# Kernel tuning notes

Hardware: AMD Instinct MI355X
Metric: run time of the kernel (lower is better)

## Reference

```python
import jax, jax.numpy as jnp
import numpy as np

# Production-scale dims (see shape_source): time-major, batch must be 1.
T, B, D, S, O, M = 1024, 1, 2048, 1024, 512, 48
TANH_BOUND = 10.0
LN_EPS = 1e-5  # haiku LayerNorm default eps


def setup_inputs() -> dict:
    key = jax.random.key(0)
    ks = jax.random.split(key, 8)

    def lin(k, fin, fout):
        return (jax.random.normal(k, (fin, fout), jnp.float32) / np.float32(np.sqrt(fin)))

    lstm_in = D + 2 * O + S  # concat([inp, error, prev_label]) then concat with h
    return {
        "inputs": jax.random.normal(ks[0], (T, B, D), jnp.float32),
        "labels": jax.random.normal(ks[1], (T, B, O), jnp.float32),
        "W_lstm": lin(ks[2], lstm_in, 4 * S),
        "b_lstm": jnp.zeros((4 * S,), jnp.float32),
        "W_write": lin(ks[3], S, 3 * M + 1),
        "b_write": jnp.zeros((3 * M + 1,), jnp.float32),
        "W_read": lin(ks[4], S, 2 * M),
        "b_read": jnp.zeros((2 * M,), jnp.float32),
        "W_rproj": lin(ks[5], M, S),
        "b_rproj": jnp.zeros((S,), jnp.float32),
        "W_out": lin(ks[6], S, O),
        "b_out": jnp.zeros((O,), jnp.float32),
    }


def _fw_memory(inputs, labels, W_lstm, b_lstm, W_write, b_write,
               W_read, b_read, W_rproj, b_rproj, W_out, b_out):
    Bsz = inputs.shape[1]  # must be 1 (jnp.outer key construction)
    slow = W_lstm.shape[1] // 4
    out_size = W_out.shape[1]
    mem = W_rproj.shape[0]

    h0 = jnp.zeros((Bsz, slow), inputs.dtype)
    c0 = jnp.zeros((Bsz, slow), inputs.dtype)
    mem0 = jnp.zeros((mem, mem * mem), inputs.dtype)
    err0 = jnp.zeros((Bsz, out_size), inputs.dtype)
    lab0 = jnp.zeros((Bsz, out_size), inputs.dtype)

    def tick(carry, x):
        h, c, memory, error, prev_label = carry
        inp, label = x  # [B,D], [B,O]
        # --- LSTM (haiku: forget bias +1) ---
        z = jnp.concatenate([inp, error, prev_label], axis=-1)
        gates = jnp.concatenate([z, h], axis=-1) @ W_lstm + b_lstm  # [B,4S]
        i, g, f, o = jnp.split(gates, 4, axis=-1)
        c = jax.nn.sigmoid(f + 1.0) * c + jax.nn.sigmoid(i) * jnp.tanh(g)
        h = jax.nn.sigmoid(o) * jnp.tanh(c)
        out = h
        # --- rank-1 fast-weight write ---
        write = out @ W_write + b_write                 # [B, 3M+1]
        beta = jax.nn.sigmoid(write[:, -1])             # [B]
        k1, k2, v = jnp.split(jnp.tanh(write[:, :-1]), 3, axis=-1)  # [B,M] each
        key_vec = (k1.reshape(-1)[:, None] * k2.reshape(-1)[None, :]).reshape(-1)  # [M^2]
        v_old = memory @ key_vec                        # [M]
        delta = (v - v_old).reshape(-1)                 # [M]
        memory = memory + beta * (delta[:, None] * key_vec[None, :])
        memory = memory / jnp.maximum(1.0, jnp.linalg.norm(memory))
        # --- rank-1 read + LayerNorm (no scale/offset) ---
        r = jnp.tanh(out @ W_read + b_read)             # [B,2M]
        n, e = jnp.split(r, 2, axis=-1)
        read_key = (n.reshape(-1)[:, None] * e.reshape(-1)[None, :]).reshape(-1)  # [M^2]
        nvec = memory @ read_key                        # [M]
        nvec = (nvec - nvec.mean()) / jnp.sqrt(nvec.var() + LN_EPS)
        readout = nvec @ W_rproj + b_rproj              # [S], broadcast over batch
        out = out + readout
        out = out @ W_out + b_out                       # [B,O]
        out = jnp.tanh(out / TANH_BOUND) * TANH_BOUND
        new_error = out - label  # grad of 0.5*sum((out-label)^2) wrt out
        return (h, c, memory, new_error, label), out

    _, outputs = jax.lax.scan(tick, (h0, c0, mem0, err0, lab0), (inputs, labels))
    return outputs  # [T,B,O]


def reference(inputs, labels, W_lstm, b_lstm, W_write, b_write,
              W_read, b_read, W_rproj, b_rproj, W_out, b_out):
    return _fw_memory(inputs, labels, W_lstm, b_lstm, W_write, b_write,
                      W_read, b_read, W_rproj, b_rproj, W_out, b_out)
```

## Files before the change

### kernel.cpp

```cpp
#include <hip/hip_runtime.h>
#include <math.h>


#define TT 1024
#define DD 2048
#define SS 1024
#define OO 512
#define MM 48
#define NG 4096
#define NWG 256
#define NTHR 256
#define NC 144
#define ND 8

#define W_HP2   0
#define W_ER2   2048
#define W_WR2   3072
#define W_VP2   3584
#define W_NP2   3872
#define W_HW2   4160
#define W_UD2   5184
#define W_IVG2  5280
#define ZERO_WORDS 208256
#define W_PRE    208256
#define W_WWRT  (W_PRE + TT*NG)
#define W_WOUTT (W_WWRT + 241*SS)
#define W_WCOMB (W_WOUTT + OO*SS)
#define W_BCOMB (W_WCOMB + MM*OO)
#define W_WLRP  (W_BCOMB + OO)

typedef unsigned long long u64;

__device__ __forceinline__ u64 ld64(const u64* p) {
  return __hip_atomic_load(p, __ATOMIC_RELAXED, __HIP_MEMORY_SCOPE_AGENT);
}
__device__ __forceinline__ void st64(u64* p, u64 v) {
  __hip_atomic_store(p, v, __ATOMIC_RELAXED, __HIP_MEMORY_SCOPE_AGENT);
}
__device__ __forceinline__ u64 mkpair(float v, int tag) {
  union { float f; unsigned u; } c; c.f = v;
  return (u64)c.u | ((u64)(unsigned)tag << 32);
}
__device__ __forceinline__ float pval(u64 p) {
  union { unsigned u; float f; } c; c.u = (unsigned)p; return c.f;
}
__device__ __forceinline__ int ptag(u64 p) { return (int)(unsigned)(p >> 32); }
__device__ __forceinline__ float sigm(float x) { return 1.f / (1.f + expf(-x)); }


__global__ void build_wwrT(const float* __restrict__ Ww, const float* __restrict__ Wr,
                           float* __restrict__ wwrT) {
  int id = blockIdx.x * 256 + threadIdx.x;
  if (id < 241 * SS) {
    int d = id >> 10, s = id & 1023;
    wwrT[id] = (d < 145) ? Ww[s * 145 + d] : Wr[s * 96 + (d - 145)];
  }
}

__global__ void build_woutT(const float* __restrict__ Wo, float* __restrict__ woutT) {
  int id = blockIdx.x * 256 + threadIdx.x;
  int o = id >> 10, s = id & 1023;
  woutT[id] = Wo[s * OO + o];
}

__global__ void repack_wl(const float* __restrict__ Wl, float* __restrict__ dst) {
  int id = blockIdx.x * 256 + threadIdx.x;
  int gb = id & 3;
  int r = id >> 2;
  int l = r % 1536;
  int s = r / 1536;
  int wrow = (l < 512) ? (2048 + l) : (2560 + l);
  dst[id] = Wl[(size_t)wrow * NG + gb * 1024 + s];
}

__global__ void wcomb_kernel(const float* __restrict__ Wrp, const float* __restrict__ brp,
                             const float* __restrict__ Wo, const float* __restrict__ bo,
                             float* __restrict__ wcomb, float* __restrict__ bcomb) {
  int id = blockIdx.x * 256 + threadIdx.x;
  int a = id >> 9, o = id & 511;
  if (a < MM) {
    float acc = 0.f;
    for (int s = 0; s < SS; ++s) acc = fmaf(Wrp[a * SS + s], Wo[s * OO + o], acc);
    wcomb[a * OO + o] = acc;
  } else if (a == MM) {
    float acc = bo[o];
    for (int s = 0; s < SS; ++s) acc = fmaf(brp[s], Wo[s * OO + o], acc);
    bcomb[o] = acc;
  }
}

__global__ __launch_bounds__(256)
void pregate_gemm(const float* __restrict__ inp, const float* __restrict__ lab,
                  const float* __restrict__ Wl, const float* __restrict__ bl,
                  float* __restrict__ pre) {
  __shared__ float As[16][65];
  __shared__ float Bs[16][64];
  const int tid = threadIdx.x;
  const int j0 = blockIdx.x * 64;
  const int t0 = blockIdx.y * 64;
  const int tx = tid & 15, ty = tid >> 4;
  float acc[4][4] = {};
  for (int kc = 0; kc < 2560; kc += 16) {
    __syncthreads();
#pragma unroll
    for (int p = 0; p < 4; ++p) {
      int id = tid + p * 256;
      int r = id >> 4, kk = id & 15;
      int t = t0 + r, k = kc + kk;
      float v;
      if (k < DD) v = inp[(size_t)t * DD + k];
      else v = (t > 0) ? lab[(size_t)(t - 1) * OO + (k - DD)] : 0.f;
      As[kk][r] = v;
      int kr = id >> 6, j = id & 63;
      int k2 = kc + kr;
      int wrow = (k2 < DD) ? k2 : (512 + k2);
      Bs[kr][j] = Wl[(size_t)wrow * NG + j0 + j];
    }
    __syncthreads();
#pragma unroll
    for (int kk = 0; kk < 16; ++kk) {
      float av[4], bv[4];
#pragma unroll
      for (int i = 0; i < 4; ++i) av[i] = As[kk][ty * 4 + i];
#pragma unroll
      for (int i = 0; i < 4; ++i) bv[i] = Bs[kk][tx * 4 + i];
#pragma unroll
      for (int i = 0; i < 4; ++i)
#pragma unroll
        for (int jx = 0; jx < 4; ++jx) acc[i][jx] = fmaf(av[i], bv[jx], acc[i][jx]);
    }
  }
#pragma unroll
  for (int i = 0; i < 4; ++i) {
    int t = t0 + ty * 4 + i;
#pragma unroll
    for (int jx = 0; jx < 4; ++jx) {
      int j = j0 + tx * 4 + jx;
      pre[(size_t)t * NG + j] = acc[i][jx] + bl[j];
    }
  }
}


__global__ __launch_bounds__(NTHR, 1)
void persistent_kernel(float* ws, const float* __restrict__ labels,
                       const float* __restrict__ bwv, const float* __restrict__ brv,
                       float* __restrict__ out) {
  u64* const hp2 = (u64*)(ws + W_HP2);
  u64* const er2 = (u64*)(ws + W_ER2);
  u64* const wr2 = (u64*)(ws + W_WR2);
  u64* const vp2 = (u64*)(ws + W_VP2);
  u64* const np2 = (u64*)(ws + W_NP2);
  u64* const hw2 = (u64*)(ws + W_HW2);
  u64* const ud2 = (u64*)(ws + W_UD2);
  u64* const iv2 = (u64*)(ws + W_IVG2);
  const float* const pre = ws + W_PRE;
  const float* const wwrT = ws + W_WWRT;
  const float* const woutT = ws + W_WOUTT;
  const float* const wcomb = ws + W_WCOMB;
  const float* const bcomb = ws + W_BCOMB;

  const int w = blockIdx.x;
  const int tid = threadIdx.x;
  const int sc = tid >> 6;
  const int rl = tid & 63;
  const float4* const blk4 =
      (const float4*)(ws + W_WLRP) + (size_t)w * 6144 + (size_t)sc * 1536;

  const bool isC = (w < NC);
  const bool isD = (w >= NC && w < NC + ND);
  const int ca = w / 3, cch = w % 3;
  const int dbase = (w - NC) * 64;
  const int p_ = w - (NC + ND);

  float4 werr[8], whh[16];
#pragma unroll
  for (int it = 0; it < 8; ++it) werr[it] = blk4[rl + it * 64];
#pragma unroll
  for (int it = 0; it < 16; ++it) whh[it] = blk4[512 + rl + it * 64];

  int slot = -1;
  float wreg[16];
  float breg = 0.f;
  if (p_ >= 0) {
    int s_ = p_ * 4 + sc;
    if (s_ < 241) slot = s_;
  }
  if (slot >= 0) {
    const float* wrow = wwrT + (size_t)slot * SS;
#pragma unroll
    for (int i = 0; i < 16; ++i) wreg[i] = wrow[rl + 64 * i];
    breg = (slot < 145) ? bwv[slot] : brv[slot - 145];
  }
  const int hslot = (p_ >= 0) ? (p_ * 4 + sc) : -1;

  float creg = 0.f;
  float ah0 = 0.f, ah1 = 0.f, ah2 = 0.f, ah3 = 0.f;
  float labr = 0.f;
  float m2c = 0.f;

  __shared__ float pg2[2][16];
  __shared__ float t1[96], t2[96], s3[49];
  __shared__ float nvln_s[MM];
  __shared__ float wcl[MM * 64];
  __shared__ float Mlds[768];
  __shared__ float vps[144], nps[144], hws[64];
  __shared__ float cred[2][4];
  __shared__ float shud[2];

  if (isD) {
    for (int i = tid; i < MM * 64; i += NTHR)
      wcl[i] = wcomb[(size_t)(i >> 6) * OO + dbase + (i & 63)];
    if (tid < 64) labr = labels[dbase + tid];
  }
  float hbias = 0.f;
  if (isD && tid < 64) hbias = bcomb[dbase + tid];
  if (tid < 16)
    pg2[0][tid] = pre[(size_t)(tid >> 2) * 1024 + w * 4 + (tid & 3)];
#pragma unroll
  for (int i = 0; i < 3; ++i) Mlds[tid + i * 256] = 0.f;
  __syncthreads();

  for (int t = 0; t < TT; ++t) {
    __syncthreads();

    float ev[8];
    if (t > 0) {
      u64 pr[8];
      for (;;) {
#pragma unroll
        for (int i = 0; i < 8; ++i) pr[i] = ld64(er2 + rl + i * 64);
        int bad = 0;
#pragma unroll
        for (int i = 0; i < 8; ++i) bad |= (ptag(pr[i]) != t);
        if (!bad) break;
        __builtin_amdgcn_s_sleep(1);
      }
#pragma unroll
      for (int i = 0; i < 8; ++i) ev[i] = pval(pr[i]);
    } else {
#pragma unroll
      for (int i = 0; i < 8; ++i) ev[i] = 0.f;
    }
    {
      float a0 = ah0, a1 = ah1, a2 = ah2, a3 = ah3;
#pragma unroll
      for (int it = 0; it < 8; ++it) {
        float xv = ev[it];
        a0 = fmaf(xv, werr[it].x, a0);
        a1 = fmaf(xv, werr[it].y, a1);
        a2 = fmaf(xv, werr[it].z, a2);
        a3 = fmaf(xv, werr[it].w, a3);
      }
#pragma unroll
      for (int off = 32; off; off >>= 1) {
        a0 += __shfl_down(a0, off, 64);
        a1 += __shfl_down(a1, off, 64);
        a2 += __shfl_down(a2, off, 64);
        a3 += __shfl_down(a3, off, 64);
      }
      if (rl == 0) {
        const float* pgc = pg2[t & 1];
        float gi = a0 + pgc[0 + sc];
        float gg = a1 + pgc[4 + sc];
        float gf = a2 + pgc[8 + sc];
        float go = a3 + pgc[12 + sc];
        creg = sigm(gf + 1.f) * creg + sigm(gi) * tanhf(gg);
        float hn = sigm(go) * tanhf(creg);
        st64(hp2 + w * 4 + sc, mkpair(hn, t + 1));
      }
    }

    if (isC) {
      if (t > 0) {
        if (tid == 0) {
          u64 pu = ld64(ud2 + ca), pv = ld64(iv2);
          while (ptag(pu) != t || ptag(pv) != t) {
            __builtin_amdgcn_s_sleep(1);
            pu = ld64(ud2 + ca); pv = ld64(iv2);
          }
          shud[0] = pval(pu); shud[1] = pval(pv);
        }
        __syncthreads();
        float uda = shud[0], ivgr = shud[1];
#pragma unroll
        for (int i = 0; i < 3; ++i) {
          int c = tid + i * 256;
          int gc = cch * 768 + c;
          int a2 = gc / 48, b2 = gc - a2 * 48;
          Mlds[c] = Mlds[c] * ivgr + uda * (t1[a2] * t1[48 + b2]);
        }
      }
      float hv[16];
      {
        u64 ph[16];
        for (;;) {
#pragma unroll
          for (int i = 0; i < 16; ++i) ph[i] = ld64(hp2 + rl + i * 64);
          int bad = 0;
#pragma unroll
          for (int i = 0; i < 16; ++i) bad |= (ptag(ph[i]) != t + 1);
          if (!bad) break;
          __builtin_amdgcn_s_sleep(1);
        }
#pragma unroll
        for (int i = 0; i < 16; ++i) hv[i] = pval(ph[i]);
      }
      __syncthreads();
      if (tid < 192) {
        int di = (tid < 96) ? tid : (tid + 49);
        u64 pr = ld64(wr2 + di);
        while (ptag(pr) != t + 1) {
          __builtin_amdgcn_s_sleep(2);
          pr = ld64(wr2 + di);
        }
        if (tid < 96) t1[tid] = pval(pr); else t2[tid - 96] = pval(pr);
      }
      __syncthreads();
      {
        float sk = 0.f, sr = 0.f;
#pragma unroll
        for (int i = 0; i < 3; ++i) {
          int c = tid + i * 256;
          int gc = cch * 768 + c;
          int a2 = gc / 48, b2 = gc - a2 * 48;
          float m = Mlds[c];
          sk = fmaf(m, t1[a2] * t1[48 + b2], sk);
          sr = fmaf(m, t2[a2] * t2[48 + b2], sr);
        }
#pragma unroll
        for (int off = 32; off; off >>= 1) {
          sk += __shfl_down(sk, off, 64);
          sr += __shfl_down(sr, off, 64);
        }
        if (rl == 0) { cred[0][sc] = sk; cred[1][sc] = sr; }
        __syncthreads();
        if (tid == 0) {
          st64(vp2 + ca * 3 + cch,
               mkpair(cred[0][0] + cred[0][1] + cred[0][2] + cred[0][3], t + 1));
          st64(np2 + ca * 3 + cch,
               mkpair(cred[1][0] + cred[1][1] + cred[1][2] + cred[1][3], t + 1));
        }
      }
      {
        float b0 = 0.f, b1 = 0.f, b2 = 0.f, b3 = 0.f;
#pragma unroll
        for (int it = 0; it < 16; ++it) {
          float xv = hv[it];
          b0 = fmaf(xv, whh[it].x, b0);
          b1 = fmaf(xv, whh[it].y, b1);
          b2 = fmaf(xv, whh[it].z, b2);
          b3 = fmaf(xv, whh[it].w, b3);
        }
        ah0 = b0; ah1 = b1; ah2 = b2; ah3 = b3;
      }
      if (tid < 16 && t + 1 < TT)
        pg2[(t + 1) & 1][tid] =
            pre[(size_t)(t + 1) * NG + (tid >> 2) * 1024 + w * 4 + (tid & 3)];
    } else if (isD) {
      float hv[16];
      {
        u64 ph[16];
        for (;;) {
#pragma unroll
          for (int i = 0; i < 16; ++i) ph[i] = ld64(hp2 + rl + i * 64);
          int bad = 0;
#pragma unroll
          for (int i = 0; i < 16; ++i) bad |= (ptag(ph[i]) != t + 1);
          if (!bad) break;
          __builtin_amdgcn_s_sleep(1);
        }
#pragma unroll
        for (int i = 0; i < 16; ++i) hv[i] = pval(ph[i]);
      }
      {
        float b0 = 0.f, b1 = 0.f, b2 = 0.f, b3 = 0.f;
#pragma unroll
        for (int it = 0; it < 16; ++it) {
          float xv = hv[it];
          b0 = fmaf(xv, whh[it].x, b0);
          b1 = fmaf(xv, whh[it].y, b1);
          b2 = fmaf(xv, whh[it].z, b2);
          b3 = fmaf(xv, whh[it].w, b3);
        }
        ah0 = b0; ah1 = b1; ah2 = b2; ah3 = b3;
      }
      if (tid < 16 && t + 1 < TT)
        pg2[(t + 1) & 1][tid] =
            pre[(size_t)(t + 1) * NG + (tid >> 2) * 1024 + w * 4 + (tid & 3)];
      float labr2 = 0.f;
      if (tid < 64 && t + 1 < TT)
        labr2 = labels[(size_t)(t + 1) * OO + dbase + tid];
      {
        const int i0 = tid, i1 = tid + 256, i2 = tid + 512;
        const bool h1 = (i1 < 593), h2 = (i2 < 593);
        auto paddr = [&](int idx) -> u64* {
          if (idx < 241) return wr2 + idx;
          if (idx < 385) return vp2 + (idx - 241);
          if (idx < 529) return np2 + (idx - 385);
          return hw2 + dbase + (idx - 529);
        };
        u64 q0, q1 = 0, q2 = 0;
        for (;;) {
          q0 = ld64(paddr(i0));
          if (h1) q1 = ld64(paddr(i1));
          if (h2) q2 = ld64(paddr(i2));
          int bad = (ptag(q0) != t + 1);
          if (h1) bad |= (ptag(q1) != t + 1);
          if (h2) bad |= (ptag(q2) != t + 1);
          if (!bad) break;
          __builtin_amdgcn_s_sleep(1);
        }
        auto route = [&](int idx, float v) {
          if (idx < 96) t1[idx] = v;
          else if (idx < 144) s3[idx - 96] = v;
          else if (idx == 144) s3[48] = v;
          else if (idx < 241) t2[idx - 145] = v;
          else if (idx < 385) vps[idx - 241] = v;
          else if (idx < 529) nps[idx - 385] = v;
          else hws[idx - 529] = v;
        };
        route(i0, pval(q0));
        if (h1) route(i1, pval(q1));
        if (h2) route(i2, pval(q2));
      }
      __syncthreads();
      if (tid < 64) {
        const int a = tid;
        const bool va = a < MM;
        float lv = 0.f, d = 0.f, t1a = 0.f, t1b = 0.f, t2a = 0.f, t2b = 0.f;
        float ln = 0.f;
        if (va) {
          lv = vps[3 * a] + vps[3 * a + 1] + vps[3 * a + 2];
          ln = nps[3 * a] + nps[3 * a + 1] + nps[3 * a + 2];
          d = s3[a] - lv;
          t1a = t1[a]; t1b = t1[48 + a];
          t2a = t2[a]; t2b = t2[48 + a];
        }
        float beta = sigm(s3[48]);
        float sdv = va ? d * lv : 0.f;
        float sdd = va ? d * d : 0.f;
        float sk1 = va ? t1a * t1a : 0.f;
        float sk2 = va ? t1b * t1b : 0.f;
        float skn = va ? t1a * t2a : 0.f;
        float ske = va ? t1b * t2b : 0.f;
#pragma unroll
        for (int off = 32; off; off >>= 1) {
          sdv += __shfl_down(sdv, off, 64);
          sdd += __shfl_down(sdd, off, 64);
          sk1 += __shfl_down(sk1, off, 64);
          sk2 += __shfl_down(sk2, off, 64);
          skn += __shfl_down(skn, off, 64);
          ske += __shfl_down(ske, off, 64);
        }
        sdv = __shfl(sdv, 0, 64);
        sdd = __shfl(sdd, 0, 64);
        sk1 = __shfl(sk1, 0, 64);
        sk2 = __shfl(sk2, 0, 64);
        skn = __shfl(skn, 0, 64);
        ske = __shfl(ske, 0, 64);
        float n2 = m2c + 2.f * beta * sdv + beta * beta * sdd * (sk1 * sk2);
        float n2c = fmaxf(n2, 0.f);
        m2c = fminf(n2c, 1.f);
        float gam = sqrtf(n2c);
        if (gam < 1.f) gam = 1.f;
        float ivg = 1.f / gam;
        float kdr = skn * ske;
        float nv = va ? (ln + beta * d * kdr) * ivg : 0.f;
        float mean = nv, msq = nv * nv;
#pragma unroll
        for (int off = 32; off; off >>= 1) {
          mean += __shfl_down(mean, off, 64);
          msq += __shfl_down(msq, off, 64);
        }
        mean = __shfl(mean, 0, 64) * (1.f / 48.f);
        msq = __shfl(msq, 0, 64) * (1.f / 48.f);
        float rstd = rsqrtf(msq - mean * mean + 1e-5f);
        if (va) nvln_s[a] = (nv - mean) * rstd;
        if (w == NC) {
          if (va) st64(ud2 + a, mkpair(beta * ivg * d, t + 1));
          if (tid == 0) st64(iv2, mkpair(ivg, t + 1));
        }
      }
      __syncthreads();
      if (tid < 64) {
        float acc = hws[tid] + hbias;
#pragma unroll 8
        for (int a = 0; a < MM; ++a) acc = fmaf(nvln_s[a], wcl[a * 64 + tid], acc);
        float y = 10.f * tanhf(acc * 0.1f);
        out[(size_t)t * OO + dbase + tid] = y;
        st64(er2 + dbase + tid, mkpair(y - labr, t + 1));
      }
      labr = labr2;
    } else {
      float hv[16];
      {
        u64 ph[16];
        for (;;) {
#pragma unroll
          for (int i = 0; i < 16; ++i) ph[i] = ld64(hp2 + rl + i * 64);
          int bad = 0;
#pragma unroll
          for (int i = 0; i < 16; ++i) bad |= (ptag(ph[i]) != t + 1);
          if (!bad) break;
          __builtin_amdgcn_s_sleep(1);
        }
#pragma unroll
        for (int i = 0; i < 16; ++i) hv[i] = pval(ph[i]);
      }
      if (slot >= 0) {
        float acc = 0.f;
#pragma unroll
        for (int i = 0; i < 16; ++i) acc = fmaf(hv[i], wreg[i], acc);
#pragma unroll
        for (int off = 32; off; off >>= 1) acc += __shfl_down(acc, off, 64);
        if (rl == 0) {
          float dv = acc + breg;
          st64(wr2 + slot, mkpair((slot == 144) ? dv : tanhf(dv), t + 1));
        }
      }
      {
        const float* wrow = woutT + (size_t)hslot * SS;
        float acc = 0.f;
#pragma unroll
        for (int i = 0; i < 16; ++i)
          acc = fmaf(hv[i], wrow[rl + i * 64], acc);
#pragma unroll
        for (int off = 32; off; off >>= 1) acc += __shfl_down(acc, off, 64);
        if (rl == 0) st64(hw2 + hslot, mkpair(acc, t + 1));
        if (hslot < 96) {
          int o2 = hslot + 416;
          const float* wrow2 = woutT + (size_t)o2 * SS;
          float ac2 = 0.f;
#pragma unroll
          for (int i = 0; i < 16; ++i)
            ac2 = fmaf(hv[i], wrow2[rl + i * 64], ac2);
#pragma unroll
          for (int off = 32; off; off >>= 1) ac2 += __shfl_down(ac2, off, 64);
          if (rl == 0) st64(hw2 + o2, mkpair(ac2, t + 1));
        }
      }
      {
        float b0 = 0.f, b1 = 0.f, b2 = 0.f, b3 = 0.f;
#pragma unroll
        for (int it = 0; it < 16; ++it) {
          float xv = hv[it];
          b0 = fmaf(xv, whh[it].x, b0);
          b1 = fmaf(xv, whh[it].y, b1);
          b2 = fmaf(xv, whh[it].z, b2);
          b3 = fmaf(xv, whh[it].w, b3);
        }
        ah0 = b0; ah1 = b1; ah2 = b2; ah3 = b3;
      }
      if (tid < 16 && t + 1 < TT)
        pg2[(t + 1) & 1][tid] =
            pre[(size_t)(t + 1) * NG + (tid >> 2) * 1024 + w * 4 + (tid & 3)];
    }
  }
}

extern "C" void kernel_launch(void* const* d_in, const int* in_sizes, int n_in,
                              void* d_out, int out_size, void* d_ws, size_t ws_size,
                              hipStream_t stream) {
  const float* inp = (const float*)d_in[0];
  const float* lab = (const float*)d_in[1];
  const float* Wl = (const float*)d_in[2];
  const float* bl = (const float*)d_in[3];
  const float* Ww = (const float*)d_in[4];
  const float* bw = (const float*)d_in[5];
  const float* Wr = (const float*)d_in[6];
  const float* br = (const float*)d_in[7];
  const float* Wrp = (const float*)d_in[8];
  const float* brp = (const float*)d_in[9];
  const float* Wo = (const float*)d_in[10];
  const float* bo = (const float*)d_in[11];
  float* ws = (float*)d_ws;
  float* outp = (float*)d_out;
  (void)in_sizes; (void)n_in; (void)out_size; (void)ws_size;

  hipMemsetAsync(d_ws, 0, (size_t)ZERO_WORDS * 4, stream);
  hipLaunchKernelGGL(build_wwrT, dim3((241 * SS + 255) / 256), dim3(256), 0, stream,
                     Ww, Wr, ws + W_WWRT);
  hipLaunchKernelGGL(build_woutT, dim3(OO * SS / 256), dim3(256), 0, stream,
                     Wo, ws + W_WOUTT);
  hipLaunchKernelGGL(repack_wl, dim3(1536 * NG / 256), dim3(256), 0, stream,
                     Wl, ws + W_WLRP);
  hipLaunchKernelGGL(wcomb_kernel, dim3(98), dim3(256), 0, stream,
                     Wrp, brp, Wo, bo, ws + W_WCOMB, ws + W_BCOMB);
  hipLaunchKernelGGL(pregate_gemm, dim3(64, 16), dim3(256), 0, stream,
                     inp, lab, Wl, bl, ws + W_PRE);
  hipLaunchKernelGGL(persistent_kernel, dim3(NWG), dim3(NTHR), 0, stream,
                     ws, lab, bw, br, outp);
}
```

Before: 14.80 ms.

## Recompute error vector locally per workgroup and rebalance persistent roles

Every workgroup now recomputes the full 512-wide output error itself from the broadcast LayerNorm vector (48 values) and the h·W_out partials. This replaces waiting on a 512-entry error exchange published by the D workgroups. The memory-chunk workgroups shrink from 144 to 48, each holding a full 48x48 row in LDS, and the H·W_out rows are cached in registers instead of being reloaded each step. The cost is redundant per-workgroup compute, heavy register use for the 96 wcomb values per thread, and every workgroup spinning on all 512 hw2 entries each step.

```diff
diff --git a/kernel.cpp b/kernel.cpp
--- a/kernel.cpp
+++ b/kernel.cpp
@@ -10,17 +10,22 @@
 #define NG 4096
 #define NWG 256
 #define NTHR 256
-#define NC 144
-#define ND 8
+#define NC 48
+#define ND0 48
+#define NDE 56
+#define NB0 56
+#define NBE 117
+#define NH0 117
+#define NSPIN 337
 
 #define W_HP2   0
-#define W_ER2   2048
-#define W_WR2   3072
-#define W_VP2   3584
-#define W_NP2   3872
-#define W_HW2   4160
-#define W_UD2   5184
-#define W_IVG2  5280
+#define W_WR2   2048
+#define W_VP2   2560
+#define W_NP2   2656
+#define W_HW2   2752
+#define W_UD2   3776
+#define W_IVG2  3872
+#define W_NV2   3874
 #define ZERO_WORDS 208256
 #define W_PRE    208256
 #define W_WWRT  (W_PRE + TT*NG)
@@ -45,6 +50,11 @@
   union { unsigned u; float f; } c; c.u = (unsigned)p; return c.f;
 }
 __device__ __forceinline__ int ptag(u64 p) { return (int)(unsigned)(p >> 32); }
+__device__ __forceinline__ float spin1(const u64* p, int tag) {
+  u64 q = ld64(p);
+  while (ptag(q) != tag) { __builtin_amdgcn_s_sleep(1); q = ld64(p); }
+  return pval(q);
+}
 __device__ __forceinline__ float sigm(float x) { return 1.f / (1.f + expf(-x)); }
 
 
@@ -147,13 +157,13 @@
                        const float* __restrict__ bwv, const float* __restrict__ brv,
                        float* __restrict__ out) {
   u64* const hp2 = (u64*)(ws + W_HP2);
-  u64* const er2 = (u64*)(ws + W_ER2);
   u64* const wr2 = (u64*)(ws + W_WR2);
   u64* const vp2 = (u64*)(ws + W_VP2);
   u64* const np2 = (u64*)(ws + W_NP2);
   u64* const hw2 = (u64*)(ws + W_HW2);
   u64* const ud2 = (u64*)(ws + W_UD2);
   u64* const iv2 = (u64*)(ws + W_IVG2);
+  u64* const nv2 = (u64*)(ws + W_NV2);
   const float* const pre = ws + W_PRE;
   const float* const wwrT = ws + W_WWRT;
   const float* const woutT = ws + W_WOUTT;
@@ -168,85 +178,96 @@
       (const float4*)(ws + W_WLRP) + (size_t)w * 6144 + (size_t)sc * 1536;
 
   const bool isC = (w < NC);
-  const bool isD = (w >= NC && w < NC + ND);
-  const int ca = w / 3, cch = w % 3;
-  const int dbase = (w - NC) * 64;
-  const int p_ = w - (NC + ND);
+  const bool isD = (w >= ND0 && w < NDE);
+  const int dbase = (w - ND0) * 64;
 
   float4 werr[8], whh[16];
 #pragma unroll
   for (int it = 0; it < 8; ++it) werr[it] = blk4[rl + it * 64];
 #pragma unroll
   for (int it = 0; it < 16; ++it) whh[it] = blk4[512 + rl + it * 64];
+
+  float wc0[48], wc1[48];
+#pragma unroll
+  for (int a = 0; a < 48; ++a) {
+    wc0[a] = wcomb[(size_t)a * OO + tid];
+    wc1[a] = wcomb[(size_t)a * OO + tid + 256];
+  }
+  const float bc0 = bcomb[tid], bc1 = bcomb[tid + 256];
 
   int slot = -1;
   float wreg[16];
   float breg = 0.f;
-  if (p_ >= 0) {
-    int s_ = p_ * 4 + sc;
-    if (s_ < 241) slot = s_;
-  }
+  if (w >= NB0 && w < NBE) { int s_ = (w - NB0) * 4 + sc; if (s_ < 241) slot = s_; }
   if (slot >= 0) {
     const float* wrow = wwrT + (size_t)slot * SS;
 #pragma unroll
     for (int i = 0; i < 16; ++i) wreg[i] = wrow[rl + 64 * i];
     breg = (slot < 145) ? bwv[slot] : brv[slot - 145];
   }
-  const int hslot = (p_ >= 0) ? (p_ * 4 + sc) : -1;
+  int hslot = -1;
+  float wh16[16];
+  if (w >= NH0) { int s_ = (w - NH0) * 4 + sc; if (s_ < 512) hslot = s_; }
+  if (hslot >= 0) {
+    const float* wrow = woutT + (size_t)hslot * SS;
+#pragma unroll
+    for (int i = 0; i < 16; ++i) wh16[i] = wrow[rl + 64 * i];
+  }
 
   float creg = 0.f;
   float ah0 = 0.f, ah1 = 0.f, ah2 = 0.f, ah3 = 0.f;
-  float labr = 0.f;
   float m2c = 0.f;
+  float zb0 = 0.f, zb1 = 0.f;
+  float lab0 = 0.f, lab1 = 0.f;
 
   __shared__ float pg2[2][16];
+  __shared__ float errs[512];
+  __shared__ float nvl[48];
   __shared__ float t1[96], t2[96], s3[49];
-  __shared__ float nvln_s[MM];
-  __shared__ float wcl[MM * 64];
-  __shared__ float Mlds[768];
-  __shared__ float vps[144], nps[144], hws[64];
+  __shared__ float nvln_s[48];
+  __shared__ float lvs[48], lns[48];
+  __shared__ float wcl[48 * 64];
+  __shared__ float Mlds[2304];
   __shared__ float cred[2][4];
   __shared__ float shud[2];
 
   if (isD) {
-    for (int i = tid; i < MM * 64; i += NTHR)
+    for (int i = tid; i < 48 * 64; i += NTHR)
       wcl[i] = wcomb[(size_t)(i >> 6) * OO + dbase + (i & 63)];
-    if (tid < 64) labr = labels[dbase + tid];
   }
   float hbias = 0.f;
   if (isD && tid < 64) hbias = bcomb[dbase + tid];
   if (tid < 16)
     pg2[0][tid] = pre[(size_t)(tid >> 2) * 1024 + w * 4 + (tid & 3)];
-#pragma unroll
-  for (int i = 0; i < 3; ++i) Mlds[tid + i * 256] = 0.f;
+  errs[tid] = 0.f; errs[tid + 256] = 0.f;
+#pragma unroll
+  for (int i = 0; i < 9; ++i) Mlds[tid + i * 256] = 0.f;
   __syncthreads();
 
   for (int t = 0; t < TT; ++t) {
     __syncthreads();
 
-    float ev[8];
     if (t > 0) {
-      u64 pr[8];
-      for (;;) {
-#pragma unroll
-        for (int i = 0; i < 8; ++i) pr[i] = ld64(er2 + rl + i * 64);
-        int bad = 0;
-#pragma unroll
-        for (int i = 0; i < 8; ++i) bad |= (ptag(pr[i]) != t);
-        if (!bad) break;
-        __builtin_amdgcn_s_sleep(1);
-      }
-#pragma unroll
-      for (int i = 0; i < 8; ++i) ev[i] = pval(pr[i]);
-    } else {
-#pragma unroll
-      for (int i = 0; i < 8; ++i) ev[i] = 0.f;
+      if (!isD) {
+        if (tid < 48) nvl[tid] = spin1(nv2 + tid, t);
+      }
+      __syncthreads();
+      const float* nvp = isD ? nvln_s : nvl;
+      float acc0 = zb0, acc1 = zb1;
+#pragma unroll
+      for (int a = 0; a < 48; ++a) {
+        acc0 = fmaf(nvp[a], wc0[a], acc0);
+        acc1 = fmaf(nvp[a], wc1[a], acc1);
+      }
+      errs[tid] = 10.f * tanhf(acc0 * 0.1f) - lab0;
+      errs[tid + 256] = 10.f * tanhf(acc1 * 0.1f) - lab1;
+      __syncthreads();
     }
     {
       float a0 = ah0, a1 = ah1, a2 = ah2, a3 = ah3;
 #pragma unroll
       for (int it = 0; it < 8; ++it) {
-        float xv = ev[it];
+        float xv = errs[rl + it * 64];
         a0 = fmaf(xv, werr[it].x, a0);
         a1 = fmaf(xv, werr[it].y, a1);
         a2 = fmaf(xv, werr[it].z, a2);
@@ -271,27 +292,19 @@
       }
     }
 
+    float hv[16];
     if (isC) {
       if (t > 0) {
-        if (tid == 0) {
-          u64 pu = ld64(ud2 + ca), pv = ld64(iv2);
-          while (ptag(pu) != t || ptag(pv) != t) {
-            __builtin_amdgcn_s_sleep(1);
-            pu = ld64(ud2 + ca); pv = ld64(iv2);
-          }
-          shud[0] = pval(pu); shud[1] = pval(pv);
-        }
+        if (tid == 0) { shud[0] = spin1(ud2 + w, t); shud[1] = spin1(iv2, t); }
         __syncthreads();
         float uda = shud[0], ivgr = shud[1];
 #pragma unroll
-        for (int i = 0; i < 3; ++i) {
+        for (int i = 0; i < 9; ++i) {
           int c = tid + i * 256;
-          int gc = cch * 768 + c;
-          int a2 = gc / 48, b2 = gc - a2 * 48;
+          int a2 = c / 48, b2 = c - a2 * 48;
           Mlds[c] = Mlds[c] * ivgr + uda * (t1[a2] * t1[48 + b2]);
         }
       }
-      float hv[16];
       {
         u64 ph[16];
         for (;;) {
@@ -309,21 +322,16 @@
       __syncthreads();
       if (tid < 192) {
         int di = (tid < 96) ? tid : (tid + 49);
-        u64 pr = ld64(wr2 + di);
-        while (ptag(pr) != t + 1) {
-          __builtin_amdgcn_s_sleep(2);
-          pr = ld64(wr2 + di);
-        }
-        if (tid < 96) t1[tid] = pval(pr); else t2[tid - 96] = pval(pr);
+        float v = spin1(wr2 + di, t + 1);
+        if (tid < 96) t1[tid] = v; else t2[tid - 96] = v;
       }
       __syncthreads();
       {
         float sk = 0.f, sr = 0.f;
 #pragma unroll
-        for (int i = 0; i < 3; ++i) {
+        for (int i = 0; i < 9; ++i) {
           int c = tid + i * 256;
-          int gc = cch * 768 + c;
-          int a2 = gc / 48, b2 = gc - a2 * 48;
+          int a2 = c / 48, b2 = c - a2 * 48;
           float m = Mlds[c];
           sk = fmaf(m, t1[a2] * t1[48 + b2], sk);
           sr = fmaf(m, t2[a2] * t2[48 + b2], sr);
@@ -336,29 +344,11 @@
         if (rl == 0) { cred[0][sc] = sk; cred[1][sc] = sr; }
         __syncthreads();
         if (tid == 0) {
-          st64(vp2 + ca * 3 + cch,
-               mkpair(cred[0][0] + cred[0][1] + cred[0][2] + cred[0][3], t + 1));
-          st64(np2 + ca * 3 + cch,
-               mkpair(cred[1][0] + cred[1][1] + cred[1][2] + cred[1][3], t + 1));
-        }
-      }
-      {
-        float b0 = 0.f, b1 = 0.f, b2 = 0.f, b3 = 0.f;
-#pragma unroll
-        for (int it = 0; it < 16; ++it) {
-          float xv = hv[it];
-          b0 = fmaf(xv, whh[it].x, b0);
-          b1 = fmaf(xv, whh[it].y, b1);
-          b2 = fmaf(xv, whh[it].z, b2);
-          b3 = fmaf(xv, whh[it].w, b3);
-        }
-        ah0 = b0; ah1 = b1; ah2 = b2; ah3 = b3;
-      }
-      if (tid < 16 && t + 1 < TT)
-        pg2[(t + 1) & 1][tid] =
-            pre[(size_t)(t + 1) * NG + (tid >> 2) * 1024 + w * 4 + (tid & 3)];
+          st64(vp2 + w, mkpair(cred[0][0] + cred[0][1] + cred[0][2] + cred[0][3], t + 1));
+          st64(np2 + w, mkpair(cred[1][0] + cred[1][1] + cred[1][2] + cred[1][3], t + 1));
+        }
+      }
     } else if (isD) {
-      float hv[16];
       {
         u64 ph[16];
         for (;;) {
@@ -374,40 +364,19 @@
         for (int i = 0; i < 16; ++i) hv[i] = pval(ph[i]);
       }
       {
-        float b0 = 0.f, b1 = 0.f, b2 = 0.f, b3 = 0.f;
-#pragma unroll
-        for (int it = 0; it < 16; ++it) {
-          float xv = hv[it];
-          b0 = fmaf(xv, whh[it].x, b0);
-          b1 = fmaf(xv, whh[it].y, b1);
-          b2 = fmaf(xv, whh[it].z, b2);
-          b3 = fmaf(xv, whh[it].w, b3);
-        }
-        ah0 = b0; ah1 = b1; ah2 = b2; ah3 = b3;
-      }
-      if (tid < 16 && t + 1 < TT)
-        pg2[(t + 1) & 1][tid] =
-            pre[(size_t)(t + 1) * NG + (tid >> 2) * 1024 + w * 4 + (tid & 3)];
-      float labr2 = 0.f;
-      if (tid < 64 && t + 1 < TT)
-        labr2 = labels[(size_t)(t + 1) * OO + dbase + tid];
-      {
-        const int i0 = tid, i1 = tid + 256, i2 = tid + 512;
-        const bool h1 = (i1 < 593), h2 = (i2 < 593);
-        auto paddr = [&](int idx) -> u64* {
+        const int i0 = tid, i1 = tid + 256;
+        const bool h1 = (i1 < NSPIN);
+        auto paddr = [&](int idx) -> const u64* {
           if (idx < 241) return wr2 + idx;
-          if (idx < 385) return vp2 + (idx - 241);
-          if (idx < 529) return np2 + (idx - 385);
-          return hw2 + dbase + (idx - 529);
+          if (idx < 289) return vp2 + (idx - 241);
+          return np2 + (idx - 289);
         };
-        u64 q0, q1 = 0, q2 = 0;
+        u64 q0, q1 = 0;
         for (;;) {
           q0 = ld64(paddr(i0));
           if (h1) q1 = ld64(paddr(i1));
-          if (h2) q2 = ld64(paddr(i2));
           int bad = (ptag(q0) != t + 1);
           if (h1) bad |= (ptag(q1) != t + 1);
-          if (h2) bad |= (ptag(q2) != t + 1);
           if (!bad) break;
           __builtin_amdgcn_s_sleep(1);
         }
@@ -416,13 +385,11 @@
           else if (idx < 144) s3[idx - 96] = v;
           else if (idx == 144) s3[48] = v;
           else if (idx < 241) t2[idx - 145] = v;
-          else if (idx < 385) vps[idx - 241] = v;
-          else if (idx < 529) nps[idx - 385] = v;
-          else hws[idx - 529] = v;
+          else if (idx < 289) lvs[idx - 241] = v;
+          else lns[idx - 289] = v;
         };
         route(i0, pval(q0));
         if (h1) route(i1, pval(q1));
-        if (h2) route(i2, pval(q2));
       }
       __syncthreads();
       if (tid < 64) {
@@ -431,8 +398,7 @@
         float lv = 0.f, d = 0.f, t1a = 0.f, t1b = 0.f, t2a = 0.f, t2b = 0.f;
         float ln = 0.f;
         if (va) {
-          lv = vps[3 * a] + vps[3 * a + 1] + vps[3 * a + 2];
-          ln = nps[3 * a] + nps[3 * a + 1] + nps[3 * a + 2];
+          lv = lvs[a]; ln = lns[a];
           d = s3[a] - lv;
           t1a = t1[a]; t1b = t1[48 + a];
           t2a = t2[a]; t2b = t2[48 + a];
@@ -476,24 +442,25 @@
         mean = __shfl(mean, 0, 64) * (1.f / 48.f);
         msq = __shfl(msq, 0, 64) * (1.f / 48.f);
         float rstd = rsqrtf(msq - mean * mean + 1e-5f);
-        if (va) nvln_s[a] = (nv - mean) * rstd;
-        if (w == NC) {
-          if (va) st64(ud2 + a, mkpair(beta * ivg * d, t + 1));
-          if (tid == 0) st64(iv2, mkpair(ivg, t + 1));
-        }
+        if (va) {
+          float nvv = (nv - mean) * rstd;
+          if (w == ND0) {
+            st64(nv2 + a, mkpair(nvv, t + 1));
+            st64(ud2 + a, mkpair(beta * ivg * d, t + 1));
+          }
+          nvln_s[a] = nvv;
+        }
+        if (w == ND0 && tid == 0) st64(iv2, mkpair(ivg, t + 1));
       }
       __syncthreads();
       if (tid < 64) {
-        float acc = hws[tid] + hbias;
+        float hwv = spin1(hw2 + dbase + tid, t + 1);
+        float acc = hwv + hbias;
 #pragma unroll 8
         for (int a = 0; a < MM; ++a) acc = fmaf(nvln_s[a], wcl[a * 64 + tid], acc);
-        float y = 10.f * tanhf(acc * 0.1f);
-        out[(size_t)t * OO + dbase + tid] = y;
-        st64(er2 + dbase + tid, mkpair(y - labr, t + 1));
-      }
-      labr = labr2;
+        out[(size_t)t * OO + dbase + tid] = 10.f * tanhf(acc * 0.1f);
+      }
     } else {
-      float hv[16];
       {
         u64 ph[16];
         for (;;) {
@@ -519,42 +486,34 @@
           st64(wr2 + slot, mkpair((slot == 144) ? dv : tanhf(dv), t + 1));
         }
       }
-      {
-        const float* wrow = woutT + (size_t)hslot * SS;
+      if (hslot >= 0) {
         float acc = 0.f;
 #pragma unroll
-        for (int i = 0; i < 16; ++i)
-          acc = fmaf(hv[i], wrow[rl + i * 64], acc);
+        for (int i = 0; i < 16; ++i) acc = fmaf(hv[i], wh16[i], acc);
 #pragma unroll
         for (int off = 32; off; off >>= 1) acc += __shfl_down(acc, off, 64);
         if (rl == 0) st64(hw2 + hslot, mkpair(acc, t + 1));
-        if (hslot < 96) {
-          int o2 = hslot + 416;
-          const float* wrow2 = woutT + (size_t)o2 * SS;
-          float ac2 = 0.f;
-#pragma unroll
-          for (int i = 0; i < 16; ++i)
-            ac2 = fmaf(hv[i], wrow2[rl + i * 64], ac2);
-#pragma unroll
-          for (int off = 32; off; off >>= 1) ac2 += __shfl_down(ac2, off, 64);
-          if (rl == 0) st64(hw2 + o2, mkpair(ac2, t + 1));
-        }
-      }
-      {
-        float b0 = 0.f, b1 = 0.f, b2 = 0.f, b3 = 0.f;
-#pragma unroll
-        for (int it = 0; it < 16; ++it) {
-          float xv = hv[it];
-          b0 = fmaf(xv, whh[it].x, b0);
-          b1 = fmaf(xv, whh[it].y, b1);
-          b2 = fmaf(xv, whh[it].z, b2);
-          b3 = fmaf(xv, whh[it].w, b3);
-        }
-        ah0 = b0; ah1 = b1; ah2 = b2; ah3 = b3;
-      }
-      if (tid < 16 && t + 1 < TT)
+      }
+    }
+
+    if (t + 1 < TT) {
+      float b0 = 0.f, b1 = 0.f, b2 = 0.f, b3 = 0.f;
+#pragma unroll
+      for (int it = 0; it < 16; ++it) {
+        float xv = hv[it];
+        b0 = fmaf(xv, whh[it].x, b0);
+        b1 = fmaf(xv, whh[it].y, b1);
+        b2 = fmaf(xv, whh[it].z, b2);
+        b3 = fmaf(xv, whh[it].w, b3);
+      }
+      ah0 = b0; ah1 = b1; ah2 = b2; ah3 = b3;
+      if (tid < 16)
         pg2[(t + 1) & 1][tid] =
             pre[(size_t)(t + 1) * NG + (tid >> 2) * 1024 + w * 4 + (tid & 3)];
+      lab0 = labels[(size_t)t * OO + tid];
+      lab1 = labels[(size_t)t * OO + tid + 256];
+      zb0 = bc0 + spin1(hw2 + tid, t + 1);
+      zb1 = bc1 + spin1(hw2 + tid + 256, t + 1);
     }
   }
 }
```

Result: slower. 15.42 ms (+4.2%).
